# Performance work log

Measured on AMD Instinct MI355X. Metric: run time of the kernel, lower is better.

Reference implementation:

```python
import jax, jax.numpy as jnp
import numpy as np

NEG_INF = -jnp.inf


def setup_inputs() -> dict:
    key = jax.random.key(0)
    x = jax.random.normal(key, (512, 1024, 192), dtype=jnp.float32)
    return {"x": x, "kept_number": 256}


def reference(x, kept_number):
    # x: [B, N, C]; literal translation of the given Merge.forward (eval mode)
    B, N, C = x.shape
    if B <= kept_number:  # original checks x.shape[0]
        return x
    metric = jax.lax.stop_gradient(x)
    # original: metric / metric.norm(dim=1, keepdim=True)  -> norm over token dim
    metric = metric / jnp.linalg.norm(metric, axis=1, keepdims=True)
    unimp = metric[:, kept_number:]              # [B, N-k, C]
    compress_number = unimp.shape[0]             # == B (as in source)
    imp = metric[:, :kept_number]                # [B, k, C]
    sim = jnp.einsum('buc,bkc->buk', unimp, imp)  # [B, N-k, k]
    sim = sim.at[:, :, 0].set(NEG_INF)           # class_token=True
    node_idx = jnp.argmax(sim, axis=-1)          # [B, N-k], first-max like torch
    dst_idx = node_idx[:, :compress_number]      # [B, B]
    src = x[:, kept_number:][:, :compress_number]  # [B, B, C] (rows actually scattered)
    dst = x[:, :kept_number]                     # [B, k, C]
    # scatter_reduce(-2, reduce='mean', include_self=True):
    # out = (dst + sum of scattered src) / (1 + count)
    sums = jax.vmap(lambda i, s: jnp.zeros((kept_number, C), x.dtype).at[i].add(s))(dst_idx, src)
    counts = jax.vmap(lambda i: jnp.zeros((kept_number,), x.dtype).at[i].add(jnp.asarray(1, x.dtype)))(dst_idx)
    return (dst + sums) / (counts[:, :, None] + 1)
```

## Files before the change

kernel.cpp:

```cpp
#include <hip/hip_runtime.h>
#include <hip/hip_bf16.h>
#include <math.h>

#define Nn   1024
#define Cn   192
#define KEPT 256
#define COMP 512
#define UT   128
#define KT   64
#define MARGIN 4e-4f
#define WCAP 1024

typedef __attribute__((ext_vector_type(8))) _Float16 half8v;
typedef __attribute__((ext_vector_type(4))) float f32x4;

__device__ __forceinline__ unsigned encf(float f) {
    unsigned u = __float_as_uint(f);
    return (u & 0x80000000u) ? ~u : (u | 0x80000000u);
}
__device__ __forceinline__ unsigned long long cvt4(float m0, float m1, float m2, float m3) {
    unsigned short h0 = __builtin_bit_cast(unsigned short, (_Float16)m0);
    unsigned short h1 = __builtin_bit_cast(unsigned short, (_Float16)m1);
    unsigned short h2 = __builtin_bit_cast(unsigned short, (_Float16)m2);
    unsigned short h3 = __builtin_bit_cast(unsigned short, (_Float16)m3);
    return (unsigned long long)h0 | ((unsigned long long)h1 << 16)
         | ((unsigned long long)h2 << 32) | ((unsigned long long)h3 << 48);
}

__global__ __launch_bounds__(768) void norm_kernel(const float* __restrict__ x,
                                                   float* __restrict__ w,
                                                   float* __restrict__ rsw) {
    __shared__ float4 red[16][48];
    int b = blockIdx.x, t = threadIdx.x;
    int c4 = t % 48, ng = t / 48;
    const float* xb = x + (size_t)b * Nn * Cn;
    float4 s = make_float4(0.f, 0.f, 0.f, 0.f);
    for (int i = 0; i < 64; ++i) {
        float4 v = *reinterpret_cast<const float4*>(
            xb + (size_t)(ng * 64 + i) * Cn + c4 * 4);
        s.x += v.x * v.x; s.y += v.y * v.y; s.z += v.z * v.z; s.w += v.w * v.w;
    }
    red[ng][c4] = s;
    __syncthreads();
    if (t < 48) {
        float4 a = make_float4(0.f, 0.f, 0.f, 0.f);
        #pragma unroll
        for (int g = 0; g < 16; ++g) {
            float4 v = red[g][t];
            a.x += v.x; a.y += v.y; a.z += v.z; a.w += v.w;
        }
        float4 wv = make_float4(1.0f / a.x, 1.0f / a.y, 1.0f / a.z, 1.0f / a.w);
        float4 rv = make_float4(rsqrtf(a.x), rsqrtf(a.y), rsqrtf(a.z), rsqrtf(a.w));
        *reinterpret_cast<float4*>(w   + (size_t)b * Cn + t * 4) = wv;
        *reinterpret_cast<float4*>(rsw + (size_t)b * Cn + t * 4) = rv;
    }
}

__global__ __launch_bounds__(512) void sim_kernel(const float* __restrict__ x,
                                                  const float* __restrict__ w,
                                                  const float* __restrict__ rsw,
                                                  int* __restrict__ dst_idx) {
    __shared__ __align__(16) unsigned short su_h[UT * Cn];
    __shared__ __align__(16) unsigned short sk_h[KT * Cn];
    __shared__ float rl[Cn];
    __shared__ float wl[Cn];
    __shared__ float rowthr[UT];
    __shared__ unsigned long long best[UT];
    __shared__ unsigned short wlist[WCAP];
    __shared__ int nc;

    const int bi   = blockIdx.x;
    const int xcd  = bi & 7;
    const int slot = bi >> 3;
    const int b    = xcd * 64 + (slot >> 2);
    const int u0   = (slot & 3) * UT;
    const int t    = threadIdx.x;
    const float* xb = x + (size_t)b * Nn * Cn;

    if (t < Cn) { rl[t] = rsw[b * Cn + t]; wl[t] = w[b * Cn + t]; }
    if (t < UT) { rowthr[t] = INFINITY; best[t] = 0ull; }
    if (t == 0) nc = 0;
    __syncthreads();

    #pragma unroll
    for (int i = 0; i < 12; ++i) {
        int idx = t + 512 * i;
        int r = idx / 48, c4 = idx % 48;
        float4 v = *reinterpret_cast<const float4*>(
            xb + (size_t)(KEPT + u0 + r) * Cn + c4 * 4);
        unsigned long long h = cvt4(v.x * rl[c4 * 4 + 0], v.y * rl[c4 * 4 + 1],
                                    v.z * rl[c4 * 4 + 2], v.w * rl[c4 * 4 + 3]);
        int byte = r * 384 + ((c4 * 8) ^ ((r & 7) << 4));
        *reinterpret_cast<unsigned long long*>(reinterpret_cast<char*>(su_h) + byte) = h;
    }

    float4 pf[6];
    #pragma unroll
    for (int i = 0; i < 6; ++i) {
        int idx = t + 512 * i;
        int r = idx / 48, c4 = idx % 48;
        pf[i] = *reinterpret_cast<const float4*>(xb + (size_t)r * Cn + c4 * 4);
    }

    const int wv   = t >> 6;
    const int ln   = t & 63;
    const int l15  = ln & 15;
    const int hi2  = ln >> 4;
    const int akey = (l15 & 7) << 4;
    const int abase = (wv * 16 + l15) * 384;
    int bbase[4];
    #pragma unroll
    for (int j = 0; j < 4; ++j) bbase[j] = (j * 16 + l15) * 384;

    f32x4 acc[4][4];
    #pragma unroll
    for (int kt = 0; kt < 4; ++kt)
        #pragma unroll
        for (int j = 0; j < 4; ++j) acc[kt][j] = (f32x4)0.f;

    #pragma unroll
    for (int kt = 0; kt < 4; ++kt) {
        __syncthreads();
        #pragma unroll
        for (int i = 0; i < 6; ++i) {
            int idx = t + 512 * i;
            int r = idx / 48, c4 = idx % 48;
            unsigned long long h = cvt4(pf[i].x * rl[c4 * 4 + 0], pf[i].y * rl[c4 * 4 + 1],
                                        pf[i].z * rl[c4 * 4 + 2], pf[i].w * rl[c4 * 4 + 3]);
            int byte = r * 384 + ((c4 * 8) ^ ((r & 7) << 4));
            *reinterpret_cast<unsigned long long*>(reinterpret_cast<char*>(sk_h) + byte) = h;
        }
        __syncthreads();
        if (kt < 3) {
            #pragma unroll
            for (int i = 0; i < 6; ++i) {
                int idx = t + 512 * i;
                int r = idx / 48, c4 = idx % 48;
                pf[i] = *reinterpret_cast<const float4*>(
                    xb + (size_t)((kt + 1) * KT + r) * Cn + c4 * 4);
            }
        }

        #pragma unroll
        for (int ks = 0; ks < 6; ++ks) {
            int koff = (ks * 64 + hi2 * 16) ^ akey;
            half8v ah = *reinterpret_cast<const half8v*>(
                reinterpret_cast<const char*>(su_h) + abase + koff);
            #pragma unroll
            for (int j = 0; j < 4; ++j) {
                half8v bh = *reinterpret_cast<const half8v*>(
                    reinterpret_cast<const char*>(sk_h) + bbase[j] + koff);
                acc[kt][j] = __builtin_amdgcn_mfma_f32_16x16x32_f16(ah, bh, acc[kt][j], 0, 0, 0);
            }
        }
    }

    float v1[4], v2[4];
    int   i1[4];
    #pragma unroll
    for (int r = 0; r < 4; ++r) { v1[r] = -INFINITY; v2[r] = -INFINITY; i1[r] = 1; }

    #pragma unroll
    for (int kt = 0; kt < 4; ++kt)
        #pragma unroll
        for (int j = 0; j < 4; ++j) {
            int k = kt * KT + j * 16 + l15;
            #pragma unroll
            for (int r = 0; r < 4; ++r) {
                float v = acc[kt][j][r];
                if (k != 0) {
                    if (v > v1[r]) { v2[r] = v1[r]; v1[r] = v; i1[r] = k; }
                    else if (v > v2[r]) v2[r] = v;
                }
            }
        }

    #pragma unroll
    for (int r = 0; r < 4; ++r) {
        #pragma unroll
        for (int off = 1; off < 16; off <<= 1) {
            float ov1 = __shfl_xor(v1[r], off);
            int   oi1 = __shfl_xor(i1[r], off);
            float ov2 = __shfl_xor(v2[r], off);
            if (ov1 > v1[r] || (ov1 == v1[r] && oi1 < i1[r])) {
                v2[r] = fmaxf(v1[r], ov2);
                v1[r] = ov1; i1[r] = oi1;
            } else {
                v2[r] = fmaxf(v2[r], ov1);
            }
        }
    }

    if (l15 == 0) {
        #pragma unroll
        for (int r = 0; r < 4; ++r) {
            int ur = wv * 16 + hi2 * 4 + r;
            if (v1[r] - v2[r] > MARGIN) dst_idx[b * COMP + u0 + ur] = i1[r];
            else rowthr[ur] = v1[r] - MARGIN;
        }
    }
    __syncthreads();

    #pragma unroll
    for (int kt = 0; kt < 4; ++kt)
        #pragma unroll
        for (int j = 0; j < 4; ++j) {
            int k = kt * KT + j * 16 + l15;
            if (k == 0) continue;
            #pragma unroll
            for (int r = 0; r < 4; ++r) {
                int ur = wv * 16 + hi2 * 4 + r;
                if (acc[kt][j][r] >= rowthr[ur]) {
                    int pos = atomicAdd(&nc, 1);
                    if (pos < WCAP)
                        wlist[pos] = (unsigned short)((ur << 8) | k);
                }
            }
        }
    __syncthreads();

    int n = nc < WCAP ? nc : WCAP;
    for (int ci = wv; ci < n; ci += 8) {
        unsigned item = wlist[ci];
        int ur = item >> 8, k = item & 255;
        const float* xu = xb + (size_t)(KEPT + u0 + ur) * Cn;
        const float* xk = xb + (size_t)k * Cn;
        float p = 0.f;
        if (ln < 48) {
            float4 a  = *reinterpret_cast<const float4*>(xu + ln * 4);
            float4 b4 = *reinterpret_cast<const float4*>(xk + ln * 4);
            p = a.x * b4.x * wl[ln * 4 + 0] + a.y * b4.y * wl[ln * 4 + 1]
              + a.z * b4.z * wl[ln * 4 + 2] + a.w * b4.w * wl[ln * 4 + 3];
        }
        #pragma unroll
        for (int off = 32; off >= 1; off >>= 1) p += __shfl_xor(p, off);
        if (ln == 0) {
            unsigned long long e = ((unsigned long long)encf(p) << 32)
                                 | (unsigned long long)(0xFFFFFFFFu - (unsigned)k);
            atomicMax(&best[ur], e);
        }
    }
    __syncthreads();

    if (t < UT && rowthr[t] < 3.0e38f) {
        unsigned k = 0xFFFFFFFFu - (unsigned)(best[t] & 0xFFFFFFFFull);
        dst_idx[b * COMP + u0 + t] = (int)k;
    }
}

__global__ __launch_bounds__(512) void merge_kernel(const float* __restrict__ x,
                                                    const int* __restrict__ dst_idx,
                                                    float* __restrict__ out) {
    __shared__ int sidx[COMP];
    __shared__ int cnt[KEPT];
    __shared__ int off[KEPT];
    __shared__ int fill[KEPT];
    __shared__ unsigned short list[COMP];

    int b = blockIdx.x, t = threadIdx.x;

    if (t < KEPT) { cnt[t] = 0; fill[t] = 0; }
    sidx[t] = dst_idx[b * COMP + t];
    __syncthreads();
    atomicAdd(&cnt[sidx[t]], 1);
    __syncthreads();

    if (t < KEPT) off[t] = cnt[t];
    __syncthreads();
    #pragma unroll
    for (int d = 1; d < KEPT; d <<= 1) {
        int v = 0;
        if (t < KEPT && t >= d) v = off[t - d];
        __syncthreads();
        if (t < KEPT) off[t] += v;
        __syncthreads();
    }

    {
        int k = sidx[t];
        int pos = off[k] - cnt[k] + atomicAdd(&fill[k], 1);
        list[pos] = (unsigned short)t;
    }
    __syncthreads();

    const float* xb   = x   + (size_t)b * Nn * Cn;
    float*       outb = out + (size_t)b * KEPT * Cn;
    const int wv  = t >> 6, ln = t & 63;
    const int qtr = ln >> 4;
    const int cq  = ln & 15;

    for (int pass = 0; pass < 8; ++pass) {
        int k = pass * 32 + wv * 4 + qtr;
        int e = off[k], c = cnt[k], s0 = e - c;
        const float* xr = xb + (size_t)k * Cn;
        float4 a0 = *reinterpret_cast<const float4*>(xr + cq * 4);
        float4 a1 = *reinterpret_cast<const float4*>(xr + (cq + 16) * 4);
        float4 a2 = *reinterpret_cast<const float4*>(xr + (cq + 32) * 4);
        for (int i = s0; i < e; ++i) {
            const float* xs = xb + (size_t)(KEPT + list[i]) * Cn;
            float4 v0  = *reinterpret_cast<const float4*>(xs + cq * 4);
            float4 v1v = *reinterpret_cast<const float4*>(xs + (cq + 16) * 4);
            float4 v2v = *reinterpret_cast<const float4*>(xs + (cq + 32) * 4);
            a0.x += v0.x;  a0.y += v0.y;  a0.z += v0.z;  a0.w += v0.w;
            a1.x += v1v.x; a1.y += v1v.y; a1.z += v1v.z; a1.w += v1v.w;
            a2.x += v2v.x; a2.y += v2v.y; a2.z += v2v.z; a2.w += v2v.w;
        }
        float rc = 1.0f / ((float)c + 1.0f);
        float* orow = outb + (size_t)k * Cn;
        *reinterpret_cast<float4*>(orow + cq * 4) =
            make_float4(a0.x * rc, a0.y * rc, a0.z * rc, a0.w * rc);
        *reinterpret_cast<float4*>(orow + (cq + 16) * 4) =
            make_float4(a1.x * rc, a1.y * rc, a1.z * rc, a1.w * rc);
        *reinterpret_cast<float4*>(orow + (cq + 32) * 4) =
            make_float4(a2.x * rc, a2.y * rc, a2.z * rc, a2.w * rc);
    }
}

extern "C" void kernel_launch(void* const* d_in, const int* in_sizes, int n_in,
                              void* d_out, int out_size, void* d_ws, size_t ws_size,
                              hipStream_t stream) {
    const float* x = (const float*)d_in[0];
    float* out = (float*)d_out;

    char* ws = (char*)d_ws;
    float* w       = (float*)ws;
    float* rsw     = (float*)(ws + (size_t)512 * Cn * 4);
    int*   dst_idx = (int*)  (ws + (size_t)2 * 512 * Cn * 4);

    norm_kernel<<<dim3(512), dim3(768), 0, stream>>>(x, w, rsw);
    sim_kernel<<<dim3(2048), dim3(512), 0, stream>>>(x, w, rsw, dst_idx);
    merge_kernel<<<dim3(512), dim3(512), 0, stream>>>(x, dst_idx, out);
}
```

Before: 251.5 us.

## Hoist A fragments to registers, use a shuffle scan, and split the merge grid

```diff
diff --git a/kernel.cpp b/kernel.cpp
--- a/kernel.cpp
+++ b/kernel.cpp
@@ -9,7 +9,7 @@
 #define UT   128
 #define KT   64
 #define MARGIN 4e-4f
-#define WCAP 1024
+#define WCAP 512
 
 typedef __attribute__((ext_vector_type(8))) _Float16 half8v;
 typedef __attribute__((ext_vector_type(4))) float f32x4;
@@ -112,6 +112,16 @@
     #pragma unroll
     for (int j = 0; j < 4; ++j) bbase[j] = (j * 16 + l15) * 384;
 
+    __syncthreads();
+
+    half8v ahr[6];
+    #pragma unroll
+    for (int ks = 0; ks < 6; ++ks) {
+        int koff = (ks * 64 + hi2 * 16) ^ akey;
+        ahr[ks] = *reinterpret_cast<const half8v*>(
+            reinterpret_cast<const char*>(su_h) + abase + koff);
+    }
+
     f32x4 acc[4][4];
     #pragma unroll
     for (int kt = 0; kt < 4; ++kt)
@@ -120,7 +130,6 @@
 
     #pragma unroll
     for (int kt = 0; kt < 4; ++kt) {
-        __syncthreads();
         #pragma unroll
         for (int i = 0; i < 6; ++i) {
             int idx = t + 512 * i;
@@ -144,15 +153,14 @@
         #pragma unroll
         for (int ks = 0; ks < 6; ++ks) {
             int koff = (ks * 64 + hi2 * 16) ^ akey;
-            half8v ah = *reinterpret_cast<const half8v*>(
-                reinterpret_cast<const char*>(su_h) + abase + koff);
             #pragma unroll
             for (int j = 0; j < 4; ++j) {
                 half8v bh = *reinterpret_cast<const half8v*>(
                     reinterpret_cast<const char*>(sk_h) + bbase[j] + koff);
-                acc[kt][j] = __builtin_amdgcn_mfma_f32_16x16x32_f16(ah, bh, acc[kt][j], 0, 0, 0);
-            }
-        }
+                acc[kt][j] = __builtin_amdgcn_mfma_f32_16x16x32_f16(ahr[ks], bh, acc[kt][j], 0, 0, 0);
+            }
+        }
+        __syncthreads();
     }
 
     float v1[4], v2[4];
@@ -253,11 +261,12 @@
                                                     float* __restrict__ out) {
     __shared__ int sidx[COMP];
     __shared__ int cnt[KEPT];
-    __shared__ int off[KEPT];
+    __shared__ int offp[KEPT];
     __shared__ int fill[KEPT];
     __shared__ unsigned short list[COMP];
-
-    int b = blockIdx.x, t = threadIdx.x;
+    __shared__ int wsum[4];
+
+    int b = blockIdx.x, half = blockIdx.y, t = threadIdx.x;
 
     if (t < KEPT) { cnt[t] = 0; fill[t] = 0; }
     sidx[t] = dst_idx[b * COMP + t];
@@ -265,20 +274,30 @@
     atomicAdd(&cnt[sidx[t]], 1);
     __syncthreads();
 
-    if (t < KEPT) off[t] = cnt[t];
-    __syncthreads();
-    #pragma unroll
-    for (int d = 1; d < KEPT; d <<= 1) {
-        int v = 0;
-        if (t < KEPT && t >= d) v = off[t - d];
-        __syncthreads();
-        if (t < KEPT) off[t] += v;
-        __syncthreads();
-    }
+    int v = 0;
+    if (t < KEPT) {
+        v = cnt[t];
+        int lane = t & 63;
+        #pragma unroll
+        for (int off = 1; off < 64; off <<= 1) {
+            int u = __shfl_up(v, off);
+            if (lane >= off) v += u;
+        }
+        if (lane == 63) wsum[t >> 6] = v;
+    }
+    __syncthreads();
+    if (t < KEPT) {
+        int wid = t >> 6;
+        if (wid > 0) v += wsum[0];
+        if (wid > 1) v += wsum[1];
+        if (wid > 2) v += wsum[2];
+        offp[t] = v;
+    }
+    __syncthreads();
 
     {
         int k = sidx[t];
-        int pos = off[k] - cnt[k] + atomicAdd(&fill[k], 1);
+        int pos = offp[k] - cnt[k] + atomicAdd(&fill[k], 1);
         list[pos] = (unsigned short)t;
     }
     __syncthreads();
@@ -289,9 +308,9 @@
     const int qtr = ln >> 4;
     const int cq  = ln & 15;
 
-    for (int pass = 0; pass < 8; ++pass) {
-        int k = pass * 32 + wv * 4 + qtr;
-        int e = off[k], c = cnt[k], s0 = e - c;
+    for (int pass = 0; pass < 4; ++pass) {
+        int k = half * 128 + pass * 32 + wv * 4 + qtr;
+        int e = offp[k], c = cnt[k], s0 = e - c;
         const float* xr = xb + (size_t)k * Cn;
         float4 a0 = *reinterpret_cast<const float4*>(xr + cq * 4);
         float4 a1 = *reinterpret_cast<const float4*>(xr + (cq + 16) * 4);
@@ -329,5 +348,5 @@
 
     norm_kernel<<<dim3(512), dim3(768), 0, stream>>>(x, w, rsw);
     sim_kernel<<<dim3(2048), dim3(512), 0, stream>>>(x, w, rsw, dst_idx);
-    merge_kernel<<<dim3(512), dim3(512), 0, stream>>>(x, dst_idx, out);
-}
+    merge_kernel<<<dim3(512, 2), dim3(512), 0, stream>>>(x, dst_idx, out);
+}
```

After: 304.3 us. +21.0%, slower.
